# Optimization experiments

Measured on AMD Instinct MI355X. Metric: run time of the kernel, lower is better.

Reference implementation:

```python
import jax, jax.numpy as jnp
import numpy as np

B, SV, SA, D, H, L, F = 1, 2048, 512, 1024, 16, 2, 4096
DH = D // H
S = SV + SA


def layer_norm(x):
    mu = jnp.mean(x, axis=-1, keepdims=True)
    var = jnp.var(x, axis=-1, keepdims=True)
    return (x - mu) * jax.lax.rsqrt(var + 1e-6)


def rms_norm(x, g):
    return x * jax.lax.rsqrt(jnp.mean(x * x, axis=-1, keepdims=True) + 1e-6) * g


def rope(x, theta):
    # x: [B,S,H*DH], theta: [S, DH//2] angles; complex-pair rotation as in rope_apply
    b, s, _ = x.shape
    x4 = x.reshape(b, s, H, DH)
    xe, xo = x4[..., 0::2], x4[..., 1::2]
    c = jnp.cos(theta)[None, :, None, :]
    sn = jnp.sin(theta)[None, :, None, :]
    re = xe * c - xo * sn
    im = xe * sn + xo * c
    return jnp.stack([re, im], axis=-1).reshape(b, s, H * DH)


def setup_inputs() -> dict:
    key = jax.random.key(0)
    ks = jax.random.split(key, 20)
    w = 0.02
    inp = {
        'video_tokens': jax.random.normal(ks[0], (B, SV, D), jnp.float32),
        'action_tokens': jax.random.normal(ks[1], (B, SA, D), jnp.float32),
        'video_freqs': jax.random.uniform(ks[2], (SV, DH // 2), jnp.float32) * 6.28,
        'action_freqs': jax.random.uniform(ks[3], (SA, DH // 2), jnp.float32) * 6.28,
        'video_t_mod': jax.random.normal(ks[4], (B, 6, D), jnp.float32),
        'action_t_mod': jax.random.normal(ks[5], (B, 6, D), jnp.float32),
        'Wq': jax.random.normal(ks[6], (2, L, D, D), jnp.float32) * w,
        'Wk': jax.random.normal(ks[7], (2, L, D, D), jnp.float32) * w,
        'Wv': jax.random.normal(ks[8], (2, L, D, D), jnp.float32) * w,
        'Wo': jax.random.normal(ks[9], (2, L, D, D), jnp.float32) * w,
        'bq': jnp.zeros((2, L, D), jnp.float32),
        'bk': jnp.zeros((2, L, D), jnp.float32),
        'bv': jnp.zeros((2, L, D), jnp.float32),
        'bo': jnp.zeros((2, L, D), jnp.float32),
        'gq': jnp.ones((2, L, D), jnp.float32),
        'gk': jnp.ones((2, L, D), jnp.float32),
        'mod': jax.random.normal(ks[10], (2, L, 6, D), jnp.float32) * 0.02,
        'W1': jax.random.normal(ks[11], (2, L, D, F), jnp.float32) * w,
        'b1': jnp.zeros((2, L, F), jnp.float32),
        'W2': jax.random.normal(ks[12], (2, L, F, D), jnp.float32) * w,
        'b2': jnp.zeros((2, L, D), jnp.float32),
    }
    # Mixed-modality ctx_mask: video bidirectional; action attends video + causal over action
    m = np.zeros((S, S), dtype=bool)
    m[:SV, :SV] = True
    m[SV:, :SV] = True
    m[SV:, SV:] = np.tril(np.ones((SA, SA), dtype=bool))
    inp['attention_mask'] = jnp.asarray(m)
    return inp


def _mot_forward(video_tokens, action_tokens, video_freqs, action_freqs,
                 video_t_mod, action_t_mod, Wq, Wk, Wv, Wo, bq, bk, bv, bo,
                 gq, gk, mod, W1, b1, W2, b2, attention_mask):
    xs = [video_tokens, action_tokens]
    thetas = [video_freqs, action_freqs]
    tmods = [video_t_mod, action_t_mod]
    scale = 1.0 / jnp.sqrt(jnp.asarray(DH, xs[0].dtype))
    for l in range(L):
        qs, kss, vs, posts = [], [], [], []
        for e in range(2):
            m6 = mod[e, l][None] + tmods[e]  # [B,6,D]
            sh_msa, sc_msa, g_msa, sh_mlp, sc_mlp, g_mlp = (
                m6[:, i:i + 1, :] for i in range(6))
            a = layer_norm(xs[e]) * (1.0 + sc_msa) + sh_msa
            q = rope(rms_norm(a @ Wq[e, l] + bq[e, l], gq[e, l]), thetas[e])
            k = rope(rms_norm(a @ Wk[e, l] + bk[e, l], gk[e, l]), thetas[e])
            v = a @ Wv[e, l] + bv[e, l]
            qs.append(q); kss.append(k); vs.append(v)
            posts.append((g_msa, sh_mlp, sc_mlp, g_mlp))
        qc = jnp.concatenate(qs, axis=1).reshape(B, S, H, DH)
        kc = jnp.concatenate(kss, axis=1).reshape(B, S, H, DH)
        vc = jnp.concatenate(vs, axis=1).reshape(B, S, H, DH)
        scores = jnp.einsum('bqhd,bkhd->bhqk', qc, kc) * scale
        scores = jnp.where(attention_mask[None, None], scores, -1e9)
        p = jax.nn.softmax(scores, axis=-1)
        o = jnp.einsum('bhqk,bkhd->bqhd', p, vc).reshape(B, S, H * DH)
        outs = [o[:, :SV], o[:, SV:]]
        for e in range(2):
            g_msa, sh_mlp, sc_mlp, g_mlp = posts[e]
            x = xs[e] + g_msa * (outs[e] @ Wo[e, l] + bo[e, l])
            mi = layer_norm(x) * (1.0 + sc_mlp) + sh_mlp
            h = jax.nn.gelu(mi @ W1[e, l] + b1[e, l], approximate=True) @ W2[e, l] + b2[e, l]
            xs[e] = x + g_mlp * h
    return jnp.concatenate(xs, axis=1)  # [B, SV+SA, D]


def reference(video_tokens, action_tokens, video_freqs, action_freqs,
              video_t_mod, action_t_mod, Wq, Wk, Wv, Wo, bq, bk, bv, bo,
              gq, gk, mod, W1, b1, W2, b2, attention_mask):
    return _mot_forward(video_tokens, action_tokens, video_freqs, action_freqs,
                        video_t_mod, action_t_mod, Wq, Wk, Wv, Wo, bq, bk, bv, bo,
                        gq, gk, mod, W1, b1, W2, b2, attention_mask)
```

## Files before the change

kernel.cpp:

```cpp
#include <hip/hip_runtime.h>
#include <hip/hip_bf16.h>

#define BF16 __hip_bfloat16
typedef short bf16x8 __attribute__((ext_vector_type(8)));
typedef float f32x4  __attribute__((ext_vector_type(4)));
typedef unsigned int u32;

#define MFMA16(a, b, c) __builtin_amdgcn_mfma_f32_16x16x32_bf16(a, b, c, 0, 0, 0)


__device__ __forceinline__ void async16(const void* g, void* l) {
  __builtin_amdgcn_global_load_lds(
      (const __attribute__((address_space(1))) u32*)g,
      (__attribute__((address_space(3))) u32*)l, 16, 0, 0);
}

__device__ __forceinline__ u32 pkbf(float a, float b) {
  union { BF16 h; unsigned short s; } ua, ub;
  ua.h = __float2bfloat16(a); ub.h = __float2bfloat16(b);
  return (u32)ua.s | ((u32)ub.s << 16);
}

__global__ __launch_bounds__(256) void wtrans(const float* __restrict__ W,
                                              BF16* __restrict__ WT, int K, int N,
                                              size_t outZ) {
  __shared__ float t[32][33];
  const float* Wm = W + (size_t)K * N * blockIdx.z;
  BF16* Tm = WT + outZ * blockIdx.z;
  int n0 = blockIdx.x * 32, k0 = blockIdx.y * 32;
  int tx = threadIdx.x & 31, ty = threadIdx.x >> 5;
#pragma unroll
  for (int i = 0; i < 4; i++)
    t[ty + 8 * i][tx] = Wm[(size_t)(k0 + ty + 8 * i) * N + n0 + tx];
  __syncthreads();
#pragma unroll
  for (int i = 0; i < 4; i++)
    Tm[(size_t)(n0 + ty + 8 * i) * K + k0 + tx] = __float2bfloat16(t[tx][ty + 8 * i]);
}

__global__ __launch_bounds__(256) void packb(const float* __restrict__ bq,
                                             const float* __restrict__ bk,
                                             const float* __restrict__ bv,
                                             float* __restrict__ bqkv) {
  int i = blockIdx.x * 256 + threadIdx.x;
  int s = i / 3072, c = i - s * 3072;
  float v = (c < 1024) ? bq[s * 1024 + c]
          : (c < 2048) ? bk[s * 1024 + c - 1024]
                       : bv[s * 1024 + c - 2048];
  bqkv[i] = v;
}

__global__ __launch_bounds__(256) void ln_mod(const float* __restrict__ x,
                                              BF16* __restrict__ out,
                                              const float* __restrict__ mod,
                                              const float* __restrict__ tmv,
                                              const float* __restrict__ tma,
                                              int l, int ish, int isc) {
  int r = blockIdx.x;
  int e = (r >= 2048) ? 1 : 0;
  const float* tm = e ? tma : tmv;
  const float* mo = mod + (size_t)((e * 2 + l) * 6) * 1024;
  float4 v = ((const float4*)(x + (size_t)r * 1024))[threadIdx.x];
  float s = v.x + v.y + v.z + v.w;
  float s2 = v.x * v.x + v.y * v.y + v.z * v.z + v.w * v.w;
#pragma unroll
  for (int off = 32; off >= 1; off >>= 1) {
    s += __shfl_down(s, off);
    s2 += __shfl_down(s2, off);
  }
  __shared__ float red[8];
  int lane = threadIdx.x & 63, w = threadIdx.x >> 6;
  if (lane == 0) { red[w] = s; red[4 + w] = s2; }
  __syncthreads();
  s = red[0] + red[1] + red[2] + red[3];
  s2 = red[4] + red[5] + red[6] + red[7];
  float mu = s * (1.f / 1024.f);
  float var = s2 * (1.f / 1024.f) - mu * mu;
  float inv = rsqrtf(var + 1e-6f);
  int c = threadIdx.x * 4;
  BF16* o = out + (size_t)r * 1024 + c;
  float xv[4] = {v.x, v.y, v.z, v.w};
#pragma unroll
  for (int k = 0; k < 4; k++) {
    float sc = mo[isc * 1024 + c + k] + tm[isc * 1024 + c + k];
    float sh = mo[ish * 1024 + c + k] + tm[ish * 1024 + c + k];
    o[k] = __float2bfloat16((xv[k] - mu) * inv * (1.f + sc) + sh);
  }
}

__global__ __launch_bounds__(256) void qk_post(const float* __restrict__ qkv,
                                               const float* __restrict__ gq,
                                               const float* __restrict__ gk,
                                               BF16* __restrict__ Qb, BF16* __restrict__ Kb,
                                               const float* __restrict__ vfreq,
                                               const float* __restrict__ afreq, int l) {
  int r = blockIdx.x;
  int which = blockIdx.y;
  const float* src = qkv + (size_t)r * 3072 + which * 1024;
  int e = (r >= 2048) ? 1 : 0;
  const float* g = (which ? gk : gq) + (size_t)(e * 2 + l) * 1024;
  BF16* dst = which ? Kb : Qb;
  const float* fr = e ? (afreq + (size_t)(r - 2048) * 32) : (vfreq + (size_t)r * 32);
  float4 v = ((const float4*)src)[threadIdx.x];
  float s2 = v.x * v.x + v.y * v.y + v.z * v.z + v.w * v.w;
#pragma unroll
  for (int off = 32; off >= 1; off >>= 1) s2 += __shfl_down(s2, off);
  __shared__ float red[4];
  int lane = threadIdx.x & 63, w = threadIdx.x >> 6;
  if (lane == 0) red[w] = s2;
  __syncthreads();
  s2 = red[0] + red[1] + red[2] + red[3];
  float inv = rsqrtf(s2 * (1.f / 1024.f) + 1e-6f);
  if (which == 0) inv *= 0.125f * 1.44269504f;
  int c = threadIdx.x * 4;
  float xe0 = v.x * inv * g[c], xo0 = v.y * inv * g[c + 1];
  float xe1 = v.z * inv * g[c + 2], xo1 = v.w * inv * g[c + 3];
  int p0 = (c & 63) >> 1;
  float c0, s0, c1, s1;
  __sincosf(fr[p0], &s0, &c0);
  __sincosf(fr[p0 + 1], &s1, &c1);
  int h = c >> 6;
  size_t o = ((size_t)h * 2560 + r) * 64 + (c & 63);
  dst[o + 0] = __float2bfloat16(xe0 * c0 - xo0 * s0);
  dst[o + 1] = __float2bfloat16(xe0 * s0 + xo0 * c0);
  dst[o + 2] = __float2bfloat16(xe1 * c1 - xo1 * s1);
  dst[o + 3] = __float2bfloat16(xe1 * s1 + xo1 * c1);
}

__global__ __launch_bounds__(256) void vpost(const float* __restrict__ qkv,
                                             BF16* __restrict__ VT) {
  __shared__ float t[32][33];
  int r0 = blockIdx.x * 32, c0 = blockIdx.y * 32;
  int tx = threadIdx.x & 31, ty = threadIdx.x >> 5;
#pragma unroll
  for (int i = 0; i < 4; i++)
    t[ty + 8 * i][tx] = qkv[(size_t)(r0 + ty + 8 * i) * 3072 + 2048 + c0 + tx];
  __syncthreads();
#pragma unroll
  for (int i = 0; i < 4; i++)
    VT[(size_t)(c0 + ty + 8 * i) * 2560 + r0 + tx] = __float2bfloat16(t[tx][ty + 8 * i]);
}

template <int EPI, int KS>
__global__ __launch_bounds__(256) void gemm2(const BF16* __restrict__ A,
                                             const BF16* __restrict__ Bw, size_t Bestride,
                                             const float* __restrict__ bias, int biasE,
                                             void* __restrict__ out, float* __restrict__ part,
                                             int N, int K) {
  __shared__ BF16 As[128 * 64];
  __shared__ BF16 Bs[128 * 64];
  int flat = blockIdx.x + blockIdx.y * gridDim.x;
  int xcd = flat & 7, slot = flat >> 3;
  int bx = slot % gridDim.x;
  int by = (slot / gridDim.x) * 8 + xcd;
  int m0 = bx * 128, n0 = by * 128;
  int e = (m0 >= 2048);
  const BF16* Ab = A + (size_t)m0 * K;
  const BF16* Bb = Bw + (e ? Bestride : 0) + (size_t)n0 * K;
  int kz0 = blockIdx.z * (K / KS), kz1 = kz0 + K / KS;
  int tid = threadIdx.x, lane = tid & 63, w = tid >> 6;
  int wr = w & 1, wc = w >> 1;
  int m15 = lane & 15, q4 = lane >> 4;
  int L[4], rS[4], cS[4];
#pragma unroll
  for (int i = 0; i < 4; i++) {
    L[i] = w * 256 + i * 64 + lane;
    rS[i] = L[i] >> 3;
    cS[i] = (L[i] & 7) ^ (rS[i] & 7);
  }
  f32x4 acc[4][4] = {};
  for (int k0 = kz0; k0 < kz1; k0 += 64) {
    __syncthreads();
#pragma unroll
    for (int i = 0; i < 4; i++) {
      async16(Ab + (size_t)rS[i] * K + k0 + cS[i] * 8, &As[L[i] * 8]);
      async16(Bb + (size_t)rS[i] * K + k0 + cS[i] * 8, &Bs[L[i] * 8]);
    }
    __syncthreads();
#pragma unroll
    for (int kk = 0; kk < 2; kk++) {
      int pos = ((kk * 4 + q4) ^ (m15 & 7)) * 8;
      bf16x8 af[4], bv[4];
#pragma unroll
      for (int i = 0; i < 4; i++) af[i] = *(const bf16x8*)&As[(wr * 64 + i * 16 + m15) * 64 + pos];
#pragma unroll
      for (int j = 0; j < 4; j++) bv[j] = *(const bf16x8*)&Bs[(wc * 64 + j * 16 + m15) * 64 + pos];
#pragma unroll
      for (int i = 0; i < 4; i++)
#pragma unroll
        for (int j = 0; j < 4; j++)
          acc[i][j] = MFMA16(af[i], bv[j], acc[i][j]);
    }
  }
#pragma unroll
  for (int i = 0; i < 4; i++) {
    int row = m0 + wr * 64 + 16 * i + q4 * 4;
#pragma unroll
    for (int j = 0; j < 4; j++) {
      int col = n0 + wc * 64 + 16 * j + m15;
      float b = (EPI == 3) ? 0.f : bias[e * biasE + col];
#pragma unroll
      for (int rg = 0; rg < 4; rg++) {
        float v = acc[i][j][rg] + b;
        size_t idx = (size_t)(row + rg) * N + col;
        if (EPI == 0) {
          ((float*)out)[idx] = v;
        } else if (EPI == 1) {
          float u = v * (0.7978845608f + 0.0356774081f * v * v);
          float d = 1.f + exp2f(-2.8853900818f * u);
          ((BF16*)out)[idx] = __float2bfloat16(v * __builtin_amdgcn_rcpf(d));
        } else {
          part[(size_t)blockIdx.z * 2560 * N + idx] = v;
        }
      }
    }
  }
}

template <int KS>
__global__ __launch_bounds__(256) void combine(const float* __restrict__ part,
                                               const float* __restrict__ biasL,
                                               const float* __restrict__ modp, int gi, int l,
                                               const float* __restrict__ tmv,
                                               const float* __restrict__ tma,
                                               const float* __restrict__ xin,
                                               float* __restrict__ xout) {
  int r = blockIdx.x, e = (r >= 2048) ? 1 : 0;
  int c = threadIdx.x * 4;
  float4 s = {0.f, 0.f, 0.f, 0.f};
#pragma unroll
  for (int z = 0; z < KS; z++) {
    float4 p = *(const float4*)&part[((size_t)z * 2560 + r) * 1024 + c];
    s.x += p.x; s.y += p.y; s.z += p.z; s.w += p.w;
  }
  float4 b = *(const float4*)&biasL[e * 2048 + c];
  const float* tm = e ? tma : tmv;
  float4 gm = *(const float4*)&modp[(size_t)((e * 2 + l) * 6 + gi) * 1024 + c];
  float4 gt = *(const float4*)&tm[gi * 1024 + c];
  float4 xi = *(const float4*)&xin[(size_t)r * 1024 + c];
  float4 o;
  o.x = xi.x + (gm.x + gt.x) * (s.x + b.x);
  o.y = xi.y + (gm.y + gt.y) * (s.y + b.y);
  o.z = xi.z + (gm.z + gt.z) * (s.z + b.z);
  o.w = xi.w + (gm.w + gt.w) * (s.w + b.w);
  *(float4*)&xout[(size_t)r * 1024 + c] = o;
}

__global__ __launch_bounds__(256) void flash5(const BF16* __restrict__ Qb,
                                              const BF16* __restrict__ Kb,
                                              const BF16* __restrict__ VT,
                                              float* __restrict__ OpA,
                                              float* __restrict__ OpB,
                                              float* __restrict__ ml) {
  const int S = 2560;
  const size_t ZO = 16ull * 40 * 4096;
  const size_t ZM = 16ull * 40 * 128;
  __shared__ BF16 Ks[2][64 * 64];
  __shared__ BF16 Vs[2][64 * 64];
  __shared__ BF16 Ps[4][16 * 64];
  int tid = threadIdx.x, lane = tid & 63, w = tid >> 6;
  int h = blockIdx.y, q0 = blockIdx.x * 64, kz = blockIdx.z;
  int m15 = lane & 15, q4 = lane >> 4;
  int actq = (q0 >= 2048);
  int nt = actq ? ((q0 >> 6) + 1) : 32;
  int tb = (kz * nt) >> 2, te = ((kz + 1) * nt) >> 2;
  const BF16* qrow = Qb + ((size_t)h * S + q0 + w * 16 + m15) * 64;
  bf16x8 qf0 = *(const bf16x8*)(qrow + q4 * 8);
  bf16x8 qf1 = *(const bf16x8*)(qrow + 32 + q4 * 8);
  const BF16* kbase = Kb + (size_t)h * S * 64;
  const BF16* vbase = VT + (size_t)h * 64 * S;
  int L0 = w * 128 + lane, L1 = L0 + 64;
  int r0 = L0 >> 3, c0 = (L0 & 7) ^ (r0 & 7);
  int r1 = L1 >> 3, c1 = (L1 & 7) ^ (r1 & 7);
  {
    const BF16* kg = kbase + (size_t)tb * 64 * 64;
    const BF16* vg = vbase + (size_t)tb * 64;
    async16(kg + (size_t)r0 * 64 + c0 * 8, &Ks[0][L0 * 8]);
    async16(kg + (size_t)r1 * 64 + c1 * 8, &Ks[0][L1 * 8]);
    async16(vg + (size_t)r0 * S + c0 * 8, &Vs[0][L0 * 8]);
    async16(vg + (size_t)r1 * S + c1 * 8, &Vs[0][L1 * 8]);
  }
  f32x4 oa[4] = {};
  float m_i = -1e30f, l_i = 0.f;
  int colq = q0 + w * 16 + m15;
  char* Pw = (char*)&Ps[w][0];
  int prow = m15 * 128;
  int pswz = (m15 & 7) << 4;
  int x0 = (q4 ^ (m15 & 7)) * 8, x1 = ((4 + q4) ^ (m15 & 7)) * 8;
  __syncthreads();
  for (int t = tb; t < te; t++) {
    int cur = (t - tb) & 1;
    if (t + 1 < te) {
      int nb = cur ^ 1;
      const BF16* kg = kbase + (size_t)(t + 1) * 64 * 64;
      const BF16* vg = vbase + (size_t)(t + 1) * 64;
      async16(kg + (size_t)r0 * 64 + c0 * 8, &Ks[nb][L0 * 8]);
      async16(kg + (size_t)r1 * 64 + c1 * 8, &Ks[nb][L1 * 8]);
      async16(vg + (size_t)r0 * S + c0 * 8, &Vs[nb][L0 * 8]);
      async16(vg + (size_t)r1 * S + c1 * 8, &Vs[nb][L1 * 8]);
    }
    f32x4 st[4];
    __builtin_amdgcn_s_setprio(1);
#pragma unroll
    for (int jt = 0; jt < 4; jt++) {
      int row = (jt * 16 + m15) * 64;
      bf16x8 kf0 = *(const bf16x8*)&Ks[cur][row + x0];
      bf16x8 kf1 = *(const bf16x8*)&Ks[cur][row + x1];
      f32x4 zz = {};
      zz = MFMA16(kf0, qf0, zz);
      st[jt] = MFMA16(kf1, qf1, zz);
    }
    __builtin_amdgcn_s_setprio(0);
    float mx = -1e30f;
    if (actq && t == nt - 1) {
#pragma unroll
      for (int jt = 0; jt < 4; jt++)
#pragma unroll
        for (int rg = 0; rg < 4; rg++) {
          int rowkv = t * 64 + jt * 16 + q4 * 4 + rg;
          if (rowkv > colq) st[jt][rg] = -1e30f;
          mx = fmaxf(mx, st[jt][rg]);
        }
    } else {
#pragma unroll
      for (int jt = 0; jt < 4; jt++) {
        mx = fmaxf(fmaxf(mx, st[jt][0]), st[jt][1]);
        mx = fmaxf(fmaxf(mx, st[jt][2]), st[jt][3]);
      }
    }
    if (!__all(mx <= m_i + 8.f)) {
      float m2 = fmaxf(mx, __shfl_xor(mx, 16));
      m2 = fmaxf(m2, __shfl_xor(m2, 32));
      float mn = fmaxf(m_i, m2);
      float al = exp2f(m_i - mn);
      m_i = mn;
      l_i *= al;
      float alr[4];
#pragma unroll
      for (int rg = 0; rg < 4; rg++) alr[rg] = __shfl(al, q4 * 4 + rg);
#pragma unroll
      for (int dt = 0; dt < 4; dt++)
#pragma unroll
        for (int rg = 0; rg < 4; rg++) oa[dt][rg] *= alr[rg];
    }
    float rs = 0.f;
#pragma unroll
    for (int jt = 0; jt < 4; jt++) {
      float p0 = exp2f(st[jt][0] - m_i), p1 = exp2f(st[jt][1] - m_i);
      float p2 = exp2f(st[jt][2] - m_i), p3 = exp2f(st[jt][3] - m_i);
      rs += (p0 + p1) + (p2 + p3);
      uint2 pr = {pkbf(p0, p1), pkbf(p2, p3)};
      *(uint2*)(Pw + prow + ((jt * 32 + q4 * 8) ^ pswz)) = pr;
    }
    l_i += rs;
    bf16x8 pf0 = *(const bf16x8*)(Pw + prow + ((q4 * 16) ^ pswz));
    bf16x8 pf1 = *(const bf16x8*)(Pw + prow + ((64 + q4 * 16) ^ pswz));
    __builtin_amdgcn_s_setprio(1);
#pragma unroll
    for (int dt = 0; dt < 4; dt++) {
      int vr = (dt * 16 + m15) * 64;
      bf16x8 vf0 = *(const bf16x8*)&Vs[cur][vr + x0];
      bf16x8 vf1 = *(const bf16x8*)&Vs[cur][vr + x1];
      oa[dt] = MFMA16(pf0, vf0, oa[dt]);
      oa[dt] = MFMA16(pf1, vf1, oa[dt]);
    }
    __builtin_amdgcn_s_setprio(0);
    __syncthreads();
  }
  l_i += __shfl_xor(l_i, 16);
  l_i += __shfl_xor(l_i, 32);
  float* Op = (kz < 2) ? (OpA + (size_t)kz * ZO) : (OpB + (size_t)(kz - 2) * ZO);
  size_t ob = ((size_t)h * 40 + blockIdx.x) * 4096;
#pragma unroll
  for (int dt = 0; dt < 4; dt++)
#pragma unroll
    for (int rg = 0; rg < 4; rg++)
      Op[ob + (size_t)(w * 16 + q4 * 4 + rg) * 64 + dt * 16 + m15] = oa[dt][rg];
  if (q4 == 0) {
    float* mp = ml + (size_t)kz * ZM + ((size_t)h * 40 + blockIdx.x) * 128;
    mp[w * 16 + m15] = m_i;
    mp[64 + w * 16 + m15] = l_i;
  }
}

__global__ __launch_bounds__(256) void fcomb4(const float* __restrict__ OpA,
                                              const float* __restrict__ OpB,
                                              const float* __restrict__ ml,
                                              BF16* __restrict__ O) {
  int qt = blockIdx.x, h = blockIdx.y;
  int q = threadIdx.x >> 2;
  int d0 = (threadIdx.x & 3) * 16;
  const size_t ZO = 16ull * 40 * 4096;
  const size_t ZM = 16ull * 40 * 128;
  size_t tile = (size_t)h * 40 + qt;
  size_t base = tile * 4096 + (size_t)q * 64 + d0;
  size_t mb = tile * 128 + q;
  float m[4], lv[4];
#pragma unroll
  for (int z = 0; z < 4; z++) {
    m[z] = ml[z * ZM + mb];
    lv[z] = ml[z * ZM + mb + 64];
  }
  float M = fmaxf(fmaxf(m[0], m[1]), fmaxf(m[2], m[3]));
  float wz[4];
  float den = 0.f;
#pragma unroll
  for (int z = 0; z < 4; z++) {
    wz[z] = exp2f(m[z] - M);
    den += wz[z] * lv[z];
  }
  float r = 1.f / den;
#pragma unroll
  for (int z = 0; z < 4; z++) wz[z] *= r;
  const float* P0 = OpA + base;
  const float* P1 = OpA + ZO + base;
  const float* P2 = OpB + base;
  const float* P3 = OpB + ZO + base;
  BF16* orow = O + (size_t)(qt * 64 + q) * 1024 + h * 64 + d0;
#pragma unroll
  for (int i = 0; i < 4; i++) {
    float4 a0 = *(const float4*)&P0[i * 4];
    float4 a1 = *(const float4*)&P1[i * 4];
    float4 a2 = *(const float4*)&P2[i * 4];
    float4 a3 = *(const float4*)&P3[i * 4];
    float vx = wz[0] * a0.x + wz[1] * a1.x + wz[2] * a2.x + wz[3] * a3.x;
    float vy = wz[0] * a0.y + wz[1] * a1.y + wz[2] * a2.y + wz[3] * a3.y;
    float vzv = wz[0] * a0.z + wz[1] * a1.z + wz[2] * a2.z + wz[3] * a3.z;
    float vw = wz[0] * a0.w + wz[1] * a1.w + wz[2] * a2.w + wz[3] * a3.w;
    uint2 pr = {pkbf(vx, vy), pkbf(vzv, vw)};
    *(uint2*)(orow + i * 4) = pr;
  }
}

extern "C" void kernel_launch(void* const* d_in, const int* in_sizes, int n_in,
                              void* d_out, int out_size, void* d_ws, size_t ws_size,
                              hipStream_t stream) {
  (void)in_sizes; (void)n_in; (void)out_size; (void)ws_size;
  const float* vid  = (const float*)d_in[0];
  const float* act  = (const float*)d_in[1];
  const float* vfr  = (const float*)d_in[2];
  const float* afr  = (const float*)d_in[3];
  const float* tmv  = (const float*)d_in[4];
  const float* tma  = (const float*)d_in[5];
  const float* Wq   = (const float*)d_in[6];
  const float* Wk   = (const float*)d_in[7];
  const float* Wv   = (const float*)d_in[8];
  const float* Wo   = (const float*)d_in[9];
  const float* bq   = (const float*)d_in[10];
  const float* bk   = (const float*)d_in[11];
  const float* bv   = (const float*)d_in[12];
  const float* bo   = (const float*)d_in[13];
  const float* gq   = (const float*)d_in[14];
  const float* gk   = (const float*)d_in[15];
  const float* modp = (const float*)d_in[16];
  const float* W1   = (const float*)d_in[17];
  const float* b1   = (const float*)d_in[18];
  const float* W2   = (const float*)d_in[19];
  const float* b2   = (const float*)d_in[20];

  char* p = (char*)d_ws;
  auto carve = [&](size_t bytes) {
    char* r = p;
    p += (bytes + 255) & ~(size_t)255;
    return r;
  };
  BF16* WqkvT = (BF16*)carve(4ull * 3072 * 1024 * 2);
  BF16* WoT   = (BF16*)carve(4ull * 1024 * 1024 * 2);
  BF16* W1T   = (BF16*)carve(4ull * 4096 * 1024 * 2);
  BF16* W2T   = (BF16*)carve(4ull * 1024 * 4096 * 2);
  float* bqkv = (float*)carve(4ull * 3072 * 4);
  float* x    = (float*)carve(2560ull * 1024 * 4);
  BF16* abf   = (BF16*)carve(2560ull * 1024 * 2);
  float* qkv  = (float*)carve(2560ull * 3072 * 4);
  BF16* Qb    = (BF16*)carve(2560ull * 1024 * 2);
  BF16* Kb    = (BF16*)carve(2560ull * 1024 * 2);
  float* part = qkv;
  const size_t ZO = 16ull * 40 * 4096;
  float* OpA = qkv;
  float* mlb = qkv + 2ull * ZO;
  BF16* VTb   = (BF16*)carve(2560ull * 1024 * 2);
  BF16* Obf   = (BF16*)carve(2560ull * 1024 * 2);
  BF16* mibf  = (BF16*)carve(2560ull * 1024 * 2);
  BF16* hbf   = (BF16*)carve(2560ull * 4096 * 2);
  float* OpB = (float*)hbf;

  hipMemcpyAsync(x, vid, 2048ull * 1024 * 4, hipMemcpyDeviceToDevice, stream);
  hipMemcpyAsync(x + 2048ull * 1024, act, 512ull * 1024 * 4, hipMemcpyDeviceToDevice, stream);

  const size_t S3 = 3072ull * 1024;
  wtrans<<<dim3(32, 32, 4), 256, 0, stream>>>(Wq, WqkvT, 1024, 1024, S3);
  wtrans<<<dim3(32, 32, 4), 256, 0, stream>>>(Wk, WqkvT + 1024ull * 1024, 1024, 1024, S3);
  wtrans<<<dim3(32, 32, 4), 256, 0, stream>>>(Wv, WqkvT + 2048ull * 1024, 1024, 1024, S3);
  wtrans<<<dim3(32, 32, 4), 256, 0, stream>>>(Wo, WoT, 1024, 1024, 1024ull * 1024);
  wtrans<<<dim3(128, 32, 4), 256, 0, stream>>>(W1, W1T, 1024, 4096, 4096ull * 1024);
  wtrans<<<dim3(32, 128, 4), 256, 0, stream>>>(W2, W2T, 4096, 1024, 1024ull * 4096);
  packb<<<48, 256, 0, stream>>>(bq, bk, bv, bqkv);

  for (int l = 0; l < 2; l++) {
    ln_mod<<<2560, 256, 0, stream>>>(x, abf, modp, tmv, tma, l, 0, 1);
    gemm2<0, 1><<<dim3(20, 24, 1), 256, 0, stream>>>(
        abf, WqkvT + (size_t)l * S3, 2 * S3, bqkv + l * 3072, 6144, qkv, nullptr, 3072, 1024);
    qk_post<<<dim3(2560, 2), 256, 0, stream>>>(qkv, gq, gk, Qb, Kb, vfr, afr, l);
    vpost<<<dim3(80, 32), 256, 0, stream>>>(qkv, VTb);
    flash5<<<dim3(40, 16, 4), 256, 0, stream>>>(Qb, Kb, VTb, OpA, OpB, mlb);
    fcomb4<<<dim3(40, 16), 256, 0, stream>>>(OpA, OpB, mlb, Obf);
    gemm2<3, 2><<<dim3(20, 8, 2), 256, 0, stream>>>(
        Obf, WoT + (size_t)l * 1024 * 1024, 2ull * 1024 * 1024, nullptr, 0, nullptr, part,
        1024, 1024);
    combine<2><<<2560, 256, 0, stream>>>(part, bo + l * 1024, modp, 2, l, tmv, tma, x, x);
    ln_mod<<<2560, 256, 0, stream>>>(x, mibf, modp, tmv, tma, l, 3, 4);
    gemm2<1, 1><<<dim3(20, 32, 1), 256, 0, stream>>>(
        mibf, W1T + (size_t)l * 4096 * 1024, 2ull * 4096 * 1024, b1 + l * 4096, 8192, hbf,
        nullptr, 4096, 1024);
    gemm2<3, 4><<<dim3(20, 8, 4), 256, 0, stream>>>(
        hbf, W2T + (size_t)l * 4096 * 1024, 2ull * 4096 * 1024, nullptr, 0, nullptr, part,
        1024, 4096);
    combine<4><<<2560, 256, 0, stream>>>(part, b2 + l * 1024, modp, 5, l, tmv, tma, x,
                                         (l == 1) ? (float*)d_out : x);
  }
}
```

Measured before the change: 766.9 us.

## Fuse LayerNorm into residual combine, store flash partials in bf16, merge QKV transposes

The LayerNorm+modulation step is folded into the residual combine kernels, so the updated residual is not re-read by a separate ln_mod launch. The initial device-to-device copies are dropped by reading the inputs directly. Flash-attention split-K partial outputs are staged through LDS and written as bf16 rather than fp32, roughly halving partial-output traffic. The three QKV weight transposes become one launch. Storing partials in bf16 adds a small rounding error before the split combine.

```diff
diff --git a/kernel.cpp b/kernel.cpp
--- a/kernel.cpp
+++ b/kernel.cpp
@@ -19,6 +19,12 @@
   union { BF16 h; unsigned short s; } ua, ub;
   ua.h = __float2bfloat16(a); ub.h = __float2bfloat16(b);
   return (u32)ua.s | ((u32)ub.s << 16);
+}
+
+__device__ __forceinline__ float bf2f(short s) {
+  union { float f; u32 u; } v;
+  v.u = ((u32)(unsigned short)s) << 16;
+  return v.f;
 }
 
 __global__ __launch_bounds__(256) void wtrans(const float* __restrict__ W,
@@ -36,6 +42,25 @@
 #pragma unroll
   for (int i = 0; i < 4; i++)
     Tm[(size_t)(n0 + ty + 8 * i) * K + k0 + tx] = __float2bfloat16(t[tx][ty + 8 * i]);
+}
+
+__global__ __launch_bounds__(256) void wtransq(const float* __restrict__ Wq,
+                                               const float* __restrict__ Wk,
+                                               const float* __restrict__ Wv,
+                                               BF16* __restrict__ WT) {
+  __shared__ float t[32][33];
+  int mat = blockIdx.z >> 2, ex = blockIdx.z & 3;
+  const float* Wm = (mat == 0 ? Wq : mat == 1 ? Wk : Wv) + (size_t)ex * 1024 * 1024;
+  BF16* Tm = WT + (size_t)ex * 3072 * 1024 + (size_t)mat * 1024 * 1024;
+  int n0 = blockIdx.x * 32, k0 = blockIdx.y * 32;
+  int tx = threadIdx.x & 31, ty = threadIdx.x >> 5;
+#pragma unroll
+  for (int i = 0; i < 4; i++)
+    t[ty + 8 * i][tx] = Wm[(size_t)(k0 + ty + 8 * i) * 1024 + n0 + tx];
+  __syncthreads();
+#pragma unroll
+  for (int i = 0; i < 4; i++)
+    Tm[(size_t)(n0 + ty + 8 * i) * 1024 + k0 + tx] = __float2bfloat16(t[tx][ty + 8 * i]);
 }
 
 __global__ __launch_bounds__(256) void packb(const float* __restrict__ bq,
@@ -50,7 +75,8 @@
   bqkv[i] = v;
 }
 
-__global__ __launch_bounds__(256) void ln_mod(const float* __restrict__ x,
+__global__ __launch_bounds__(256) void ln_mod(const float* __restrict__ xV,
+                                              const float* __restrict__ xA,
                                               BF16* __restrict__ out,
                                               const float* __restrict__ mod,
                                               const float* __restrict__ tmv,
@@ -58,9 +84,10 @@
                                               int l, int ish, int isc) {
   int r = blockIdx.x;
   int e = (r >= 2048) ? 1 : 0;
+  const float* xrow = e ? (xA + (size_t)(r - 2048) * 1024) : (xV + (size_t)r * 1024);
   const float* tm = e ? tma : tmv;
   const float* mo = mod + (size_t)((e * 2 + l) * 6) * 1024;
-  float4 v = ((const float4*)(x + (size_t)r * 1024))[threadIdx.x];
+  float4 v = ((const float4*)xrow)[threadIdx.x];
   float s = v.x + v.y + v.z + v.w;
   float s2 = v.x * v.x + v.y * v.y + v.z * v.z + v.w * v.w;
 #pragma unroll
@@ -217,14 +244,17 @@
   }
 }
 
-template <int KS>
-__global__ __launch_bounds__(256) void combine(const float* __restrict__ part,
-                                               const float* __restrict__ biasL,
-                                               const float* __restrict__ modp, int gi, int l,
-                                               const float* __restrict__ tmv,
-                                               const float* __restrict__ tma,
-                                               const float* __restrict__ xin,
-                                               float* __restrict__ xout) {
+template <int KS, int LN>
+__global__ __launch_bounds__(256) void combine_ln(const float* __restrict__ part,
+                                                  const float* __restrict__ biasL,
+                                                  const float* __restrict__ modp,
+                                                  int gi, int lg, int ll, int ish, int isc,
+                                                  const float* __restrict__ tmv,
+                                                  const float* __restrict__ tma,
+                                                  const float* __restrict__ xinV,
+                                                  const float* __restrict__ xinA,
+                                                  float* __restrict__ xout,
+                                                  BF16* __restrict__ lnout) {
   int r = blockIdx.x, e = (r >= 2048) ? 1 : 0;
   int c = threadIdx.x * 4;
   float4 s = {0.f, 0.f, 0.f, 0.f};
@@ -235,25 +265,52 @@
   }
   float4 b = *(const float4*)&biasL[e * 2048 + c];
   const float* tm = e ? tma : tmv;
-  float4 gm = *(const float4*)&modp[(size_t)((e * 2 + l) * 6 + gi) * 1024 + c];
+  float4 gm = *(const float4*)&modp[(size_t)((e * 2 + lg) * 6 + gi) * 1024 + c];
   float4 gt = *(const float4*)&tm[gi * 1024 + c];
-  float4 xi = *(const float4*)&xin[(size_t)r * 1024 + c];
+  const float* xrow = e ? (xinA + (size_t)(r - 2048) * 1024) : (xinV + (size_t)r * 1024);
+  float4 xi = *(const float4*)&xrow[c];
   float4 o;
   o.x = xi.x + (gm.x + gt.x) * (s.x + b.x);
   o.y = xi.y + (gm.y + gt.y) * (s.y + b.y);
   o.z = xi.z + (gm.z + gt.z) * (s.z + b.z);
   o.w = xi.w + (gm.w + gt.w) * (s.w + b.w);
   *(float4*)&xout[(size_t)r * 1024 + c] = o;
-}
-
-__global__ __launch_bounds__(256) void flash5(const BF16* __restrict__ Qb,
+  if (LN) {
+    float su = o.x + o.y + o.z + o.w;
+    float s2 = o.x * o.x + o.y * o.y + o.z * o.z + o.w * o.w;
+#pragma unroll
+    for (int off = 32; off >= 1; off >>= 1) {
+      su += __shfl_down(su, off);
+      s2 += __shfl_down(s2, off);
+    }
+    __shared__ float red[8];
+    int lane = threadIdx.x & 63, w = threadIdx.x >> 6;
+    if (lane == 0) { red[w] = su; red[4 + w] = s2; }
+    __syncthreads();
+    su = red[0] + red[1] + red[2] + red[3];
+    s2 = red[4] + red[5] + red[6] + red[7];
+    float mu = su * (1.f / 1024.f);
+    float var = s2 * (1.f / 1024.f) - mu * mu;
+    float inv = rsqrtf(var + 1e-6f);
+    const float* mo = modp + (size_t)((e * 2 + ll) * 6) * 1024;
+    BF16* ob = lnout + (size_t)r * 1024 + c;
+    float ov[4] = {o.x, o.y, o.z, o.w};
+#pragma unroll
+    for (int k = 0; k < 4; k++) {
+      float sc = mo[isc * 1024 + c + k] + tm[isc * 1024 + c + k];
+      float sh = mo[ish * 1024 + c + k] + tm[ish * 1024 + c + k];
+      ob[k] = __float2bfloat16((ov[k] - mu) * inv * (1.f + sc) + sh);
+    }
+  }
+}
+
+__global__ __launch_bounds__(256) void flash6(const BF16* __restrict__ Qb,
                                               const BF16* __restrict__ Kb,
                                               const BF16* __restrict__ VT,
-                                              float* __restrict__ OpA,
-                                              float* __restrict__ OpB,
+                                              BF16* __restrict__ Opb,
                                               float* __restrict__ ml) {
   const int S = 2560;
-  const size_t ZO = 16ull * 40 * 4096;
+  const size_t ZOb = 16ull * 40 * 4096;
   const size_t ZM = 16ull * 40 * 128;
   __shared__ BF16 Ks[2][64 * 64];
   __shared__ BF16 Vs[2][64 * 64];
@@ -369,28 +426,35 @@
   }
   l_i += __shfl_xor(l_i, 16);
   l_i += __shfl_xor(l_i, 32);
-  float* Op = (kz < 2) ? (OpA + (size_t)kz * ZO) : (OpB + (size_t)(kz - 2) * ZO);
-  size_t ob = ((size_t)h * 40 + blockIdx.x) * 4096;
-#pragma unroll
-  for (int dt = 0; dt < 4; dt++)
-#pragma unroll
-    for (int rg = 0; rg < 4; rg++)
-      Op[ob + (size_t)(w * 16 + q4 * 4 + rg) * 64 + dt * 16 + m15] = oa[dt][rg];
   if (q4 == 0) {
     float* mp = ml + (size_t)kz * ZM + ((size_t)h * 40 + blockIdx.x) * 128;
     mp[w * 16 + m15] = m_i;
     mp[64 + w * 16 + m15] = l_i;
   }
-}
-
-__global__ __launch_bounds__(256) void fcomb4(const float* __restrict__ OpA,
-                                              const float* __restrict__ OpB,
-                                              const float* __restrict__ ml,
-                                              BF16* __restrict__ O) {
+  BF16* rp = &Ks[0][0];
+#pragma unroll
+  for (int dt = 0; dt < 4; dt++)
+#pragma unroll
+    for (int rg = 0; rg < 4; rg++)
+      rp[(w * 16 + q4 * 4 + rg) * 72 + dt * 16 + m15] = __float2bfloat16(oa[dt][rg]);
+  __syncthreads();
+  BF16* Opz = Opb + (size_t)kz * ZOb + ((size_t)h * 40 + blockIdx.x) * 4096;
+#pragma unroll
+  for (int kk = 0; kk < 2; kk++) {
+    int k = tid * 2 + kk;
+    int row = k >> 3, ci = k & 7;
+    uint4 d = *(const uint4*)&rp[row * 72 + ci * 8];
+    *(uint4*)&Opz[(size_t)row * 64 + ci * 8] = d;
+  }
+}
+
+__global__ __launch_bounds__(256) void fcomb4b(const BF16* __restrict__ Opb,
+                                               const float* __restrict__ ml,
+                                               BF16* __restrict__ O) {
   int qt = blockIdx.x, h = blockIdx.y;
   int q = threadIdx.x >> 2;
   int d0 = (threadIdx.x & 3) * 16;
-  const size_t ZO = 16ull * 40 * 4096;
+  const size_t ZOb = 16ull * 40 * 4096;
   const size_t ZM = 16ull * 40 * 128;
   size_t tile = (size_t)h * 40 + qt;
   size_t base = tile * 4096 + (size_t)q * 64 + d0;
@@ -412,24 +476,24 @@
   float r = 1.f / den;
 #pragma unroll
   for (int z = 0; z < 4; z++) wz[z] *= r;
-  const float* P0 = OpA + base;
-  const float* P1 = OpA + ZO + base;
-  const float* P2 = OpB + base;
-  const float* P3 = OpB + ZO + base;
+  float acc[16] = {};
+#pragma unroll
+  for (int z = 0; z < 4; z++) {
+    const BF16* P = Opb + z * ZOb + base;
+    bf16x8 a = *(const bf16x8*)P;
+    bf16x8 b = *(const bf16x8*)(P + 8);
+#pragma unroll
+    for (int i = 0; i < 8; i++) {
+      acc[i] += wz[z] * bf2f(a[i]);
+      acc[8 + i] += wz[z] * bf2f(b[i]);
+    }
+  }
   BF16* orow = O + (size_t)(qt * 64 + q) * 1024 + h * 64 + d0;
-#pragma unroll
-  for (int i = 0; i < 4; i++) {
-    float4 a0 = *(const float4*)&P0[i * 4];
-    float4 a1 = *(const float4*)&P1[i * 4];
-    float4 a2 = *(const float4*)&P2[i * 4];
-    float4 a3 = *(const float4*)&P3[i * 4];
-    float vx = wz[0] * a0.x + wz[1] * a1.x + wz[2] * a2.x + wz[3] * a3.x;
-    float vy = wz[0] * a0.y + wz[1] * a1.y + wz[2] * a2.y + wz[3] * a3.y;
-    float vzv = wz[0] * a0.z + wz[1] * a1.z + wz[2] * a2.z + wz[3] * a3.z;
-    float vw = wz[0] * a0.w + wz[1] * a1.w + wz[2] * a2.w + wz[3] * a3.w;
-    uint2 pr = {pkbf(vx, vy), pkbf(vzv, vw)};
-    *(uint2*)(orow + i * 4) = pr;
-  }
+  u32 pk[8];
+#pragma unroll
+  for (int i = 0; i < 8; i++) pk[i] = pkbf(acc[2 * i], acc[2 * i + 1]);
+  *(uint4*)&orow[0] = *(uint4*)&pk[0];
+  *(uint4*)&orow[8] = *(uint4*)&pk[4];
 }
 
 extern "C" void kernel_launch(void* const* d_in, const int* in_sizes, int n_in,
@@ -475,47 +539,49 @@
   BF16* Qb    = (BF16*)carve(2560ull * 1024 * 2);
   BF16* Kb    = (BF16*)carve(2560ull * 1024 * 2);
   float* part = qkv;
-  const size_t ZO = 16ull * 40 * 4096;
-  float* OpA = qkv;
-  float* mlb = qkv + 2ull * ZO;
+  const size_t ZOb = 16ull * 40 * 4096;
+  BF16* Opb = (BF16*)qkv;
+  float* mlb = (float*)((char*)qkv + 4ull * ZOb * 2);
   BF16* VTb   = (BF16*)carve(2560ull * 1024 * 2);
   BF16* Obf   = (BF16*)carve(2560ull * 1024 * 2);
   BF16* mibf  = (BF16*)carve(2560ull * 1024 * 2);
   BF16* hbf   = (BF16*)carve(2560ull * 4096 * 2);
-  float* OpB = (float*)hbf;
-
-  hipMemcpyAsync(x, vid, 2048ull * 1024 * 4, hipMemcpyDeviceToDevice, stream);
-  hipMemcpyAsync(x + 2048ull * 1024, act, 512ull * 1024 * 4, hipMemcpyDeviceToDevice, stream);
 
   const size_t S3 = 3072ull * 1024;
-  wtrans<<<dim3(32, 32, 4), 256, 0, stream>>>(Wq, WqkvT, 1024, 1024, S3);
-  wtrans<<<dim3(32, 32, 4), 256, 0, stream>>>(Wk, WqkvT + 1024ull * 1024, 1024, 1024, S3);
-  wtrans<<<dim3(32, 32, 4), 256, 0, stream>>>(Wv, WqkvT + 2048ull * 1024, 1024, 1024, S3);
+  wtransq<<<dim3(32, 32, 12), 256, 0, stream>>>(Wq, Wk, Wv, WqkvT);
   wtrans<<<dim3(32, 32, 4), 256, 0, stream>>>(Wo, WoT, 1024, 1024, 1024ull * 1024);
   wtrans<<<dim3(128, 32, 4), 256, 0, stream>>>(W1, W1T, 1024, 4096, 4096ull * 1024);
   wtrans<<<dim3(32, 128, 4), 256, 0, stream>>>(W2, W2T, 4096, 1024, 1024ull * 4096);
   packb<<<48, 256, 0, stream>>>(bq, bk, bv, bqkv);
 
+  ln_mod<<<2560, 256, 0, stream>>>(vid, act, abf, modp, tmv, tma, 0, 0, 1);
+
   for (int l = 0; l < 2; l++) {
-    ln_mod<<<2560, 256, 0, stream>>>(x, abf, modp, tmv, tma, l, 0, 1);
     gemm2<0, 1><<<dim3(20, 24, 1), 256, 0, stream>>>(
         abf, WqkvT + (size_t)l * S3, 2 * S3, bqkv + l * 3072, 6144, qkv, nullptr, 3072, 1024);
     qk_post<<<dim3(2560, 2), 256, 0, stream>>>(qkv, gq, gk, Qb, Kb, vfr, afr, l);
     vpost<<<dim3(80, 32), 256, 0, stream>>>(qkv, VTb);
-    flash5<<<dim3(40, 16, 4), 256, 0, stream>>>(Qb, Kb, VTb, OpA, OpB, mlb);
-    fcomb4<<<dim3(40, 16), 256, 0, stream>>>(OpA, OpB, mlb, Obf);
+    flash6<<<dim3(40, 16, 4), 256, 0, stream>>>(Qb, Kb, VTb, Opb, mlb);
+    fcomb4b<<<dim3(40, 16), 256, 0, stream>>>(Opb, mlb, Obf);
     gemm2<3, 2><<<dim3(20, 8, 2), 256, 0, stream>>>(
         Obf, WoT + (size_t)l * 1024 * 1024, 2ull * 1024 * 1024, nullptr, 0, nullptr, part,
         1024, 1024);
-    combine<2><<<2560, 256, 0, stream>>>(part, bo + l * 1024, modp, 2, l, tmv, tma, x, x);
-    ln_mod<<<2560, 256, 0, stream>>>(x, mibf, modp, tmv, tma, l, 3, 4);
+    combine_ln<2, 1><<<2560, 256, 0, stream>>>(
+        part, bo + l * 1024, modp, 2, l, l, 3, 4, tmv, tma,
+        (l == 0) ? vid : x, (l == 0) ? act : (x + 2048ull * 1024), x, mibf);
     gemm2<1, 1><<<dim3(20, 32, 1), 256, 0, stream>>>(
         mibf, W1T + (size_t)l * 4096 * 1024, 2ull * 4096 * 1024, b1 + l * 4096, 8192, hbf,
         nullptr, 4096, 1024);
     gemm2<3, 4><<<dim3(20, 8, 4), 256, 0, stream>>>(
         hbf, W2T + (size_t)l * 4096 * 1024, 2ull * 4096 * 1024, nullptr, 0, nullptr, part,
         1024, 4096);
-    combine<4><<<2560, 256, 0, stream>>>(part, b2 + l * 1024, modp, 5, l, tmv, tma, x,
-                                         (l == 1) ? (float*)d_out : x);
-  }
-}
+    if (l == 0) {
+      combine_ln<4, 1><<<2560, 256, 0, stream>>>(
+          part, b2, modp, 5, 0, 1, 0, 1, tmv, tma, x, x + 2048ull * 1024, x, abf);
+    } else {
+      combine_ln<4, 0><<<2560, 256, 0, stream>>>(
+          part, b2 + 1024, modp, 5, 1, 0, 0, 0, tmv, tma, x, x + 2048ull * 1024,
+          (float*)d_out, nullptr);
+    }
+  }
+}
```

Result: faster. 750.9 us (-2.1%).
